# Performance work log

Measured on AMD Instinct MI355X. Metric: run time of the kernel, lower is better.

The kernel has to match this reference:

```python
import jax, jax.numpy as jnp
import numpy as np

N, E = 100000, 1600000
D_IN, D_H, D_OUT = 128, 128, 64


def setup_inputs() -> dict:
    key = jax.random.key(0)
    ks = jax.random.split(key, 9)
    features = jax.random.normal(ks[0], (N, D_IN), dtype=jnp.float32)
    src = jax.random.randint(ks[1], (E,), 0, N, dtype=jnp.int32)
    dst = jax.random.randint(ks[2], (E,), 0, N, dtype=jnp.int32)
    # GraphConv weights (glorot-ish scale)
    W1 = jax.random.normal(ks[3], (D_IN, D_H), dtype=jnp.float32) * (1.0 / np.sqrt(D_IN))
    b1 = jnp.zeros((D_H,), dtype=jnp.float32)
    W2 = jax.random.normal(ks[4], (D_H, D_H), dtype=jnp.float32) * (1.0 / np.sqrt(D_H))
    b2 = jnp.zeros((D_H,), dtype=jnp.float32)
    W3 = jax.random.normal(ks[5], (D_H, D_OUT), dtype=jnp.float32) * (1.0 / np.sqrt(D_H))
    b3 = jnp.zeros((D_OUT,), dtype=jnp.float32)
    return {"features": features, "src": src, "dst": dst,
            "W1": W1, "b1": b1, "W2": W2, "b2": b2, "W3": W3, "b3": b3}


def reference(features, src, dst, W1, b1, W2, b2, W3, b3):
    n = features.shape[0]
    ones_e = jnp.ones(src.shape[0], dtype=features.dtype)
    # DGL GraphConv norm='both': degrees clamped to min 1
    out_deg = jnp.clip(jax.ops.segment_sum(ones_e, src, num_segments=n), 1.0)
    in_deg = jnp.clip(jax.ops.segment_sum(ones_e, dst, num_segments=n), 1.0)
    norm_src = out_deg ** -0.5  # [N]
    norm_dst = in_deg ** -0.5   # [N]

    def graph_conv(h, W, b, relu):
        h = h * norm_src[:, None]                                   # D_out^{-1/2} scale
        m = jax.ops.segment_sum(h[src], dst, num_segments=n)        # SpMM aggregate
        m = m * norm_dst[:, None]                                   # D_in^{-1/2} scale
        h = m @ W + b                                               # linear
        return jax.nn.relu(h) if relu else h

    # dropout is identity in eval mode (deterministic reference)
    h = graph_conv(features, W1, b1, True)
    h = graph_conv(h, W2, b2, True)
    h = graph_conv(h, W3, b3, False)
    return jax.nn.log_softmax(h, axis=1)
```

## Files before the change

### kernel.cpp

```cpp
#include <hip/hip_runtime.h>
#include <math.h>

#define D 128
#define DO 64

#define CHUNK_BITS 15
#define CHUNK_SZ   32768
#define HWORDS     (CHUNK_SZ/4)
#define NSLICE     64

typedef unsigned int uint32;
typedef short bf8s __attribute__((ext_vector_type(8)));
typedef float f32x16 __attribute__((ext_vector_type(16)));

__device__ __forceinline__ unsigned short f2bf(float f) {
    uint32 u = __float_as_uint(f);
    u += 0x7FFFu + ((u >> 16) & 1u);
    return (unsigned short)(u >> 16);
}
__device__ __forceinline__ float bf_lo(uint32 p) { return __uint_as_float(p << 16); }
__device__ __forceinline__ float bf_hi(uint32 p) { return __uint_as_float(p & 0xFFFF0000u); }
__device__ __forceinline__ void acc2(float4& a, uint2 q) {
    a.x += bf_lo(q.x); a.y += bf_hi(q.x);
    a.z += bf_lo(q.y); a.w += bf_hi(q.y);
}

__device__ __forceinline__ f32x16 mfma32(bf8s a, bf8s b, f32x16 c) {
    return __builtin_amdgcn_mfma_f32_32x32x16_bf16(a, b, c, 0, 0, 0);
}
#define ZERO16 {0.f,0.f,0.f,0.f,0.f,0.f,0.f,0.f,0.f,0.f,0.f,0.f,0.f,0.f,0.f,0.f}

__global__ void k_pack_w(const float* __restrict__ W1, const float* __restrict__ W2,
                         const float* __restrict__ W3,
                         unsigned short* __restrict__ P1, unsigned short* __restrict__ P2,
                         unsigned short* __restrict__ P3) {
    int t = blockIdx.x * 256 + threadIdx.x;
    const float* W; unsigned short* P; int slot, NCT, ncols;
    if (t < 2048)      { W = W1; P = P1; slot = t;        NCT = 4; ncols = 128; }
    else if (t < 4096) { W = W2; P = P2; slot = t - 2048; NCT = 4; ncols = 128; }
    else if (t < 5120) { W = W3; P = P3; slot = t - 4096; NCT = 2; ncols = 64;  }
    else return;
    int lane = slot & 63, rest = slot >> 6;
    int ct = rest % NCT, ks = rest / NCT;
    int k0 = ks * 16 + (lane >> 5) * 8;
    int colidx = ct * 32 + (lane & 31);
    unsigned u[4];
#pragma unroll
    for (int b = 0; b < 4; ++b) {
        unsigned lo = f2bf(W[(size_t)(k0 + 2 * b) * ncols + colidx]);
        unsigned hi = f2bf(W[(size_t)(k0 + 2 * b + 1) * ncols + colidx]);
        u[b] = lo | (hi << 16);
    }
    ((uint4*)P)[slot] = make_uint4(u[0], u[1], u[2], u[3]);
}

__global__ __launch_bounds__(256) void k_hist_gemm1(
    const int* __restrict__ src, const int* __restrict__ dst, int E,
    int NH, int NBg, int gemmPer,
    uint32* __restrict__ histS, uint32* __restrict__ histD,
    const float* __restrict__ F, const unsigned short* __restrict__ Wp1,
    unsigned short* __restrict__ T1, int N) {
    __shared__ __align__(16) char smemraw[64 * 132 * 4];
    const int tid = threadIdx.x;
    const int P = 1 + gemmPer;
    const int per = blockIdx.x / P;
    const int pos = blockIdx.x % P;

    if (pos == 0) {
        if (per >= 2 * NH) return;
        bool isS = per >= NH;
        int h = isS ? per - NH : per;
        int chunk = h / NSLICE, slice = h % NSLICE;
        const int* key = isS ? src : dst;
        uint32* hist = (uint32*)smemraw;
        for (int w = tid; w < HWORDS; w += 256) hist[w] = 0;
        __syncthreads();
        int base = chunk << CHUNK_BITS;
        const int nE4 = E >> 2;
        int lo = (int)(((long long)slice * nE4) / NSLICE);
        int hi = (int)(((long long)(slice + 1) * nE4) / NSLICE);
        for (int idx = lo + tid; idx < hi; idx += 256) {
            int4 k4 = ((const int4*)key)[idx];
            unsigned o;
            o = (unsigned)(k4.x - base); if (o < CHUNK_SZ) atomicAdd(&hist[o >> 2], 1u << ((o & 3) * 8));
            o = (unsigned)(k4.y - base); if (o < CHUNK_SZ) atomicAdd(&hist[o >> 2], 1u << ((o & 3) * 8));
            o = (unsigned)(k4.z - base); if (o < CHUNK_SZ) atomicAdd(&hist[o >> 2], 1u << ((o & 3) * 8));
            o = (unsigned)(k4.w - base); if (o < CHUNK_SZ) atomicAdd(&hist[o >> 2], 1u << ((o & 3) * 8));
        }
        if (slice == NSLICE - 1 && tid == 0) {
            for (int i = nE4 * 4; i < E; ++i) {
                unsigned o = (unsigned)(key[i] - base);
                if (o < CHUNK_SZ) atomicAdd(&hist[o >> 2], 1u << ((o & 3) * 8));
            }
        }
        __syncthreads();
        uint32* outp = (isS ? histS : histD) + (size_t)h * HWORDS;
        for (int w = tid; w < HWORDS; w += 256) outp[w] = hist[w];
        return;
    }
    int gid = per * gemmPer + (pos - 1);
    if (gid >= NBg) return;
    const int n0 = gid * 64;
    const float4* M4 = (const float4*)F;
#pragma unroll
    for (int it = 0; it < 8; ++it) {
        int id = it * 256 + tid;
        int nl = id >> 5, k4 = id & 31;
        float4 v = make_float4(0.f, 0.f, 0.f, 0.f);
        int n = n0 + nl;
        if (n < N) v = M4[(size_t)n * 32 + k4];
        ushort4 o;
        o.x = f2bf(v.x); o.y = f2bf(v.y); o.z = f2bf(v.z); o.w = f2bf(v.w);
        *(ushort4*)(smemraw + ((unsigned)(nl * 256 + k4 * 8) ^ ((nl & 15) << 4))) = o;
    }
    __syncthreads();
    const int wid = tid >> 6, wl = tid & 63;
    const int rt = wid >> 1, ctb = (wid & 1) * 2;
    const bf8s* Wp = (const bf8s*)Wp1;
    f32x16 acc0 = ZERO16, acc1 = ZERO16;
    const int arow = rt * 32 + (wl & 31);
    const unsigned axor = (unsigned)((arow & 15) << 4);
    const unsigned abase = (unsigned)(arow * 256 + (wl >> 5) * 16);
#pragma unroll
    for (int ks = 0; ks < 8; ++ks) {
        bf8s af = *(const bf8s*)(smemraw + ((abase + ks * 32) ^ axor));
        acc0 = mfma32(af, Wp[(ks * 4 + ctb) * 64 + wl], acc0);
        acc1 = mfma32(af, Wp[(ks * 4 + ctb + 1) * 64 + wl], acc1);
    }
    const int colb = wl & 31;
    const int rbase = rt * 32 + ((wl >> 5) << 2);
#pragma unroll
    for (int reg = 0; reg < 16; ++reg) {
        int n = n0 + (reg & 3) + 8 * (reg >> 2) + rbase;
        if (n < N) {
            T1[(size_t)n * 128 + ctb * 32 + colb] = f2bf(acc0[reg]);
            T1[(size_t)n * 128 + (ctb + 1) * 32 + colb] = f2bf(acc1[reg]);
        }
    }
}

__global__ void k_merge_norms(const uint32* __restrict__ histS, uint32* __restrict__ histD,
                              int* __restrict__ degi, float* __restrict__ ns,
                              float* __restrict__ nd, int N, int NCHUNK) {
    int w = blockIdx.x * 256 + threadIdx.x;
    if (w >= NCHUNK * HWORDS) return;
    int chunk = w / HWORDS, ww = w - chunk * HWORDS;
    int n0 = (chunk << CHUNK_BITS) + ww * 4;
    if (n0 >= N) return;
    size_t basehist = ((size_t)chunk * NSLICE) * HWORDS + ww;
    uint32 runD = 0, runS = 0;
#pragma unroll 4
    for (int s = 0; s < NSLICE; ++s) {
        size_t idx = basehist + (size_t)s * HWORDS;
        uint32 c = histD[idx];
        histD[idx] = runD;
        runD += c;
        runS += histS[idx];
    }
#pragma unroll
    for (int k = 0; k < 4; ++k) {
        int n = n0 + k;
        if (n < N) {
            int dcur = (int)((runD >> (k * 8)) & 0xFF);
            int ocur = (int)((runS >> (k * 8)) & 0xFF);
            degi[n] = dcur;
            ns[n] = rsqrtf((float)(ocur < 1 ? 1 : ocur));
            nd[n] = rsqrtf((float)(dcur < 1 ? 1 : dcur));
        }
    }
}

__global__ void k_scan_block(const int* __restrict__ cnt, int* __restrict__ rp,
                             int* __restrict__ bsum, int N) {
    __shared__ int sdat[256];
    int i = blockIdx.x * 256 + threadIdx.x;
    int v = (i < N) ? cnt[i] : 0;
    sdat[threadIdx.x] = v;
    __syncthreads();
    for (int off = 1; off < 256; off <<= 1) {
        int t = (threadIdx.x >= off) ? sdat[threadIdx.x - off] : 0;
        __syncthreads();
        sdat[threadIdx.x] += t;
        __syncthreads();
    }
    if (i < N) rp[i] = sdat[threadIdx.x] - v;
    if (threadIdx.x == 255) bsum[blockIdx.x] = sdat[255];
}

__global__ void k_scan_bsum(int* __restrict__ bsum, int NB) {
    __shared__ int sdat[512];
    int tid = threadIdx.x;
    int v = (tid < NB) ? bsum[tid] : 0;
    sdat[tid] = v;
    __syncthreads();
    for (int off = 1; off < 512; off <<= 1) {
        int t = (tid >= off) ? sdat[tid - off] : 0;
        __syncthreads();
        sdat[tid] += t;
        __syncthreads();
    }
    if (tid < NB) bsum[tid] = sdat[tid] - v;
}

__global__ void k_scan_add(int* __restrict__ rp, const int* __restrict__ bsum,
                           int N, int E, uint32* __restrict__ Az, uint32* __restrict__ Bz) {
    int i = blockIdx.x * 256 + threadIdx.x;
    if (i < N) rp[i] += bsum[i >> 8];
    if (i == N) rp[N] = E;
    if (i < 64) { Az[i] = 0; Bz[i] = 0; }
}

__global__ __launch_bounds__(256) void k_scatter_rescale(
    const int* __restrict__ src, const int* __restrict__ dst, int E,
    const uint32* __restrict__ histD, const int* __restrict__ rp,
    int* __restrict__ col, int NH,
    unsigned short* __restrict__ T1, const float* __restrict__ ns, int N) {
    __shared__ uint32 cnt[HWORDS];
    const int tid = threadIdx.x;
    if (blockIdx.x >= NH) {
        int i = (blockIdx.x - NH) * 256 + tid;
        if (i < N * 32) {
            float s = ns[i >> 5];
            uint2 q = ((uint2*)T1)[i];
            ushort4 o;
            o.x = f2bf(bf_lo(q.x) * s); o.y = f2bf(bf_hi(q.x) * s);
            o.z = f2bf(bf_lo(q.y) * s); o.w = f2bf(bf_hi(q.y) * s);
            ((uint2*)T1)[i] = *(uint2*)&o;
        }
        return;
    }
    int chunk = blockIdx.x / NSLICE, slice = blockIdx.x % NSLICE;
    const uint32* Pslice = histD + ((size_t)(chunk * NSLICE + slice)) * HWORDS;
    for (int w = tid; w < HWORDS; w += 256) cnt[w] = Pslice[w];
    __syncthreads();
    int base = chunk << CHUNK_BITS;
    const int nE4 = E >> 2;
    int lo = (int)(((long long)slice * nE4) / NSLICE);
    int hi = (int)(((long long)(slice + 1) * nE4) / NSLICE);
    for (int idx = lo + tid; idx < hi; idx += 256) {
        int4 s4 = ((const int4*)src)[idx];
        int4 d4 = ((const int4*)dst)[idx];
        unsigned o;
        o = (unsigned)(d4.x - base);
        if (o < CHUNK_SZ) {
            uint32 old = atomicAdd(&cnt[o >> 2], 1u << ((o & 3) * 8));
            col[rp[d4.x] + ((old >> ((o & 3) * 8)) & 0xFF)] = s4.x;
        }
        o = (unsigned)(d4.y - base);
        if (o < CHUNK_SZ) {
            uint32 old = atomicAdd(&cnt[o >> 2], 1u << ((o & 3) * 8));
            col[rp[d4.y] + ((old >> ((o & 3) * 8)) & 0xFF)] = s4.y;
        }
        o = (unsigned)(d4.z - base);
        if (o < CHUNK_SZ) {
            uint32 old = atomicAdd(&cnt[o >> 2], 1u << ((o & 3) * 8));
            col[rp[d4.z] + ((old >> ((o & 3) * 8)) & 0xFF)] = s4.z;
        }
        o = (unsigned)(d4.w - base);
        if (o < CHUNK_SZ) {
            uint32 old = atomicAdd(&cnt[o >> 2], 1u << ((o & 3) * 8));
            col[rp[d4.w] + ((old >> ((o & 3) * 8)) & 0xFF)] = s4.w;
        }
    }
    if (slice == NSLICE - 1 && tid == 0) {
        for (int i = nE4 * 4; i < E; ++i) {
            unsigned o = (unsigned)(dst[i] - base);
            if (o < CHUNK_SZ) {
                uint32 old = atomicAdd(&cnt[o >> 2], 1u << ((o & 3) * 8));
                col[rp[dst[i]] + ((old >> ((o & 3) * 8)) & 0xFF)] = src[i];
            }
        }
    }
}


#define SPMM_SH(K) int c##K = __shfl(cvec, j + K, 32);
#define SPMM_LD(K) uint2 q##K = T2[(((unsigned)c##K) << 5) + (unsigned)lane];
#define SPMM_AC(K) acc2(((K) & 1) ? a1 : a0, q##K);

__device__ __forceinline__ float4 spmm_gather_row(
    const uint2* __restrict__ T2, const int* __restrict__ col,
    int s, int e, int cvec, int lane, int N) {
    float4 a0 = make_float4(0.f, 0.f, 0.f, 0.f), a1 = a0;
    int base = s, rem = e - s;
#pragma unroll 1
    while (rem > 0) {
        int cnt = rem < 32 ? rem : 32;
        int padded = (cnt + 7) & ~7;
        int j = 0;
#pragma unroll 1
        for (; j + 16 <= padded; j += 16) {
            SPMM_SH(0) SPMM_SH(1) SPMM_SH(2) SPMM_SH(3)
            SPMM_SH(4) SPMM_SH(5) SPMM_SH(6) SPMM_SH(7)
            SPMM_SH(8) SPMM_SH(9) SPMM_SH(10) SPMM_SH(11)
            SPMM_SH(12) SPMM_SH(13) SPMM_SH(14) SPMM_SH(15)
            SPMM_LD(0) SPMM_LD(1) SPMM_LD(2) SPMM_LD(3)
            SPMM_LD(4) SPMM_LD(5) SPMM_LD(6) SPMM_LD(7)
            SPMM_LD(8) SPMM_LD(9) SPMM_LD(10) SPMM_LD(11)
            SPMM_LD(12) SPMM_LD(13) SPMM_LD(14) SPMM_LD(15)
            SPMM_AC(0) SPMM_AC(1) SPMM_AC(2) SPMM_AC(3)
            SPMM_AC(4) SPMM_AC(5) SPMM_AC(6) SPMM_AC(7)
            SPMM_AC(8) SPMM_AC(9) SPMM_AC(10) SPMM_AC(11)
            SPMM_AC(12) SPMM_AC(13) SPMM_AC(14) SPMM_AC(15)
        }
        if (j < padded) {
            SPMM_SH(0) SPMM_SH(1) SPMM_SH(2) SPMM_SH(3)
            SPMM_SH(4) SPMM_SH(5) SPMM_SH(6) SPMM_SH(7)
            SPMM_LD(0) SPMM_LD(1) SPMM_LD(2) SPMM_LD(3)
            SPMM_LD(4) SPMM_LD(5) SPMM_LD(6) SPMM_LD(7)
            SPMM_AC(0) SPMM_AC(1) SPMM_AC(2) SPMM_AC(3)
            SPMM_AC(4) SPMM_AC(5) SPMM_AC(6) SPMM_AC(7)
        }
        base += 32; rem -= 32;
        if (rem > 0) {
            int t = base + lane;
            cvec = (t < e) ? col[t] : N;
        }
    }
    float4 r;
    r.x = a0.x + a1.x; r.y = a0.y + a1.y;
    r.z = a0.z + a1.z; r.w = a0.w + a1.w;
    return r;
}

#define A64_SH(K) int c##K = __shfl(cvec, j + K, 32);
#define A64_LD(K) uint32 q##K = Y2[(((unsigned)c##K) << 5) + (unsigned)lane];
#define A64_AC(K) { if ((K) & 1) { lo1 += bf_lo(q##K); hi1 += bf_hi(q##K); } \
                    else         { lo0 += bf_lo(q##K); hi0 += bf_hi(q##K); } }

__device__ __forceinline__ float2 agg64_gather_row(
    const uint32* __restrict__ Y2, const int* __restrict__ col,
    int s, int e, int cvec, int lane, int N) {
    float lo0 = 0.f, hi0 = 0.f, lo1 = 0.f, hi1 = 0.f;
    int base = s, rem = e - s;
#pragma unroll 1
    while (rem > 0) {
        int cnt = rem < 32 ? rem : 32;
        int padded = (cnt + 7) & ~7;
        int j = 0;
#pragma unroll 1
        for (; j + 16 <= padded; j += 16) {
            A64_SH(0) A64_SH(1) A64_SH(2) A64_SH(3)
            A64_SH(4) A64_SH(5) A64_SH(6) A64_SH(7)
            A64_SH(8) A64_SH(9) A64_SH(10) A64_SH(11)
            A64_SH(12) A64_SH(13) A64_SH(14) A64_SH(15)
            A64_LD(0) A64_LD(1) A64_LD(2) A64_LD(3)
            A64_LD(4) A64_LD(5) A64_LD(6) A64_LD(7)
            A64_LD(8) A64_LD(9) A64_LD(10) A64_LD(11)
            A64_LD(12) A64_LD(13) A64_LD(14) A64_LD(15)
            A64_AC(0) A64_AC(1) A64_AC(2) A64_AC(3)
            A64_AC(4) A64_AC(5) A64_AC(6) A64_AC(7)
            A64_AC(8) A64_AC(9) A64_AC(10) A64_AC(11)
            A64_AC(12) A64_AC(13) A64_AC(14) A64_AC(15)
        }
        if (j < padded) {
            A64_SH(0) A64_SH(1) A64_SH(2) A64_SH(3)
            A64_SH(4) A64_SH(5) A64_SH(6) A64_SH(7)
            A64_LD(0) A64_LD(1) A64_LD(2) A64_LD(3)
            A64_LD(4) A64_LD(5) A64_LD(6) A64_LD(7)
            A64_AC(0) A64_AC(1) A64_AC(2) A64_AC(3)
            A64_AC(4) A64_AC(5) A64_AC(6) A64_AC(7)
        }
        base += 32; rem -= 32;
        if (rem > 0) {
            int t = base + lane;
            cvec = (t < e) ? col[t] : N;
        }
    }
    return make_float2(lo0 + lo1, hi0 + hi1);
}

template <int JOUT>
__global__ __launch_bounds__(256) void k_spmm_gemm(
    const unsigned short* __restrict__ T, const int* __restrict__ rp,
    const int* __restrict__ col, const float* __restrict__ ns,
    const float* __restrict__ nd, const float* __restrict__ bias,
    const unsigned short* __restrict__ Wpk, unsigned short* __restrict__ out, int N) {
    __shared__ __align__(16) char MsRaw[32 * 256];
    if (JOUT == 64 && blockIdx.x == 0 && threadIdx.x < 32) {
        ((uint32*)out)[(size_t)N * 32 + threadIdx.x] = 0;
    }
    const int n0 = blockIdx.x * 32;
    const int g = threadIdx.x >> 5;
    const int lane = threadIdx.x & 31;
    const uint2* T2 = (const uint2*)T;
    float4 bv = ((const float4*)bias)[lane];

    const int row0 = n0 + (g << 2);
    int rb = 0;
    {
        int idx = row0 + lane;
        if (idx > N) idx = N;
        if (lane < 5) rb = rp[idx];
    }
    int s0 = __shfl(rb, 0, 32), s1 = __shfl(rb, 1, 32), s2 = __shfl(rb, 2, 32),
        s3 = __shfl(rb, 3, 32), s4 = __shfl(rb, 4, 32);
    int cv0 = N, cv1 = N, cv2 = N, cv3 = N;
    { int t = s0 + lane; if (t < s1) cv0 = col[t]; }
    { int t = s1 + lane; if (t < s2) cv1 = col[t]; }
    { int t = s2 + lane; if (t < s3) cv2 = col[t]; }
    { int t = s3 + lane; if (t < s4) cv3 = col[t]; }

#define SPMM_ROW_EPI(RI, SS, EE, CV) { \
    float4 t = spmm_gather_row(T2, col, SS, EE, CV, lane, N); \
    int row = row0 + RI; \
    if (row < N) { \
        float sd = nd[row], sr = ns[row]; \
        ushort4 o; \
        o.x = f2bf(fmaxf(fmaf(t.x, sd, bv.x), 0.f) * sr); \
        o.y = f2bf(fmaxf(fmaf(t.y, sd, bv.y), 0.f) * sr); \
        o.z = f2bf(fmaxf(fmaf(t.z, sd, bv.z), 0.f) * sr); \
        o.w = f2bf(fmaxf(fmaf(t.w, sd, bv.w), 0.f) * sr); \
        int lr = row - n0; \
        *(ushort4*)(MsRaw + ((unsigned)(lr * 256 + lane * 8) ^ ((lr & 15) << 4))) = o; \
    } }

    SPMM_ROW_EPI(0, s0, s1, cv0)
    SPMM_ROW_EPI(1, s1, s2, cv1)
    SPMM_ROW_EPI(2, s2, s3, cv2)
    SPMM_ROW_EPI(3, s3, s4, cv3)
#undef SPMM_ROW_EPI

    __syncthreads();
    const int wid = threadIdx.x >> 6, wl = threadIdx.x & 63;
    const int NCT = (JOUT == 128) ? 4 : 2;
    if (JOUT == 128 || wid < 2) {
        const bf8s* Wp = (const bf8s*)Wpk;
        f32x16 acc = ZERO16;
        const int arow = wl & 31;
        const unsigned axor = (unsigned)((arow & 15) << 4);
        const unsigned abase = (unsigned)(arow * 256 + (wl >> 5) * 16);
#pragma unroll
        for (int ks = 0; ks < 8; ++ks) {
            bf8s af = *(const bf8s*)(MsRaw + ((abase + ks * 32) ^ axor));
            acc = mfma32(af, Wp[(ks * NCT + wid) * 64 + wl], acc);
        }
        const int colb = wid * 32 + (wl & 31);
        const int rb2 = (wl >> 5) << 2;
#pragma unroll
        for (int reg = 0; reg < 16; ++reg) {
            int n = n0 + (reg & 3) + 8 * (reg >> 2) + rb2;
            if (n < N) out[(size_t)n * JOUT + colb] = f2bf(acc[reg]);
        }
    }
}

__global__ __launch_bounds__(256) void k_agg64_lsm(
    const unsigned short* __restrict__ Y, const int* __restrict__ rp,
    const int* __restrict__ col, const float* __restrict__ nd,
    const float* __restrict__ b3, float* __restrict__ out, int N) {
    int row = blockIdx.x * 8 + (threadIdx.x >> 5);
    if (row >= N) return;
    int lane = threadIdx.x & 31;
    const uint32* Y2 = (const uint32*)Y;
    int s = rp[row], e = rp[row + 1];
    int cv;
    { int t = s + lane; cv = (t < e) ? col[t] : N; }
    float2 agg = agg64_gather_row(Y2, col, s, e, cv, lane, N);
    float sd = nd[row];
    float2 bb = ((const float2*)b3)[lane];
    float v0 = agg.x * sd + bb.x;
    float v1 = agg.y * sd + bb.y;
    float m = fmaxf(v0, v1);
#pragma unroll
    for (int o = 16; o; o >>= 1) m = fmaxf(m, __shfl_xor(m, o, 32));
    float ex = expf(v0 - m) + expf(v1 - m);
#pragma unroll
    for (int o = 16; o; o >>= 1) ex += __shfl_xor(ex, o, 32);
    float ls = m + logf(ex);
    ((float2*)out)[(size_t)row * 32 + lane] = make_float2(v0 - ls, v1 - ls);
}

extern "C" void kernel_launch(void* const* d_in, const int* in_sizes, int n_in,
                              void* d_out, int out_size, void* d_ws, size_t ws_size,
                              hipStream_t stream) {
    const float* features = (const float*)d_in[0];
    const int*   src      = (const int*)d_in[1];
    const int*   dst      = (const int*)d_in[2];
    const float* W1       = (const float*)d_in[3];
    const float* b1       = (const float*)d_in[4];
    const float* W2       = (const float*)d_in[5];
    const float* b2       = (const float*)d_in[6];
    const float* W3       = (const float*)d_in[7];
    const float* b3       = (const float*)d_in[8];
    float* out = (float*)d_out;

    const int N = in_sizes[0] / D;
    const int E = in_sizes[1];

    const int NCHUNK = (N + CHUNK_SZ - 1) >> CHUNK_BITS;
    const int NH = NCHUNK * NSLICE;

    char* p = (char*)d_ws;
    unsigned short* A = (unsigned short*)p; p += ((size_t)N + 1) * D * sizeof(unsigned short);
    unsigned short* B = (unsigned short*)p; p += ((size_t)N + 1) * D * sizeof(unsigned short);
    int* col    = (int*)p;   p += (size_t)E * sizeof(int);
    int* rp     = (int*)p;   p += ((size_t)N + 4) * sizeof(int);
    int* degi   = (int*)p;   p += (size_t)N * sizeof(int);
    float* ns   = (float*)p; p += (size_t)N * sizeof(float);
    float* nd   = (float*)p; p += (size_t)N * sizeof(float);
    int* bsum   = (int*)p;   p += 4096 * sizeof(int);
    uint32* histS = (uint32*)p; p += (size_t)NH * HWORDS * sizeof(uint32);
    uint32* histD = (uint32*)p; p += (size_t)NH * HWORDS * sizeof(uint32);
    unsigned short* Wp1 = (unsigned short*)p; p += 16384 * sizeof(unsigned short);
    unsigned short* Wp2 = (unsigned short*)p; p += 16384 * sizeof(unsigned short);
    unsigned short* Wp3 = (unsigned short*)p; p += 8192 * sizeof(unsigned short);

    const int gN  = (N + 255) / 256;
    const int NBg = (N + 63) / 64;
    const int periods = 2 * NH;
    const int gemmPer = (NBg + periods - 1) / periods;
    const int G1 = periods * (1 + gemmPer);

    k_pack_w<<<20, 256, 0, stream>>>(W1, W2, W3, Wp1, Wp2, Wp3);
    k_hist_gemm1<<<G1, 256, 0, stream>>>(src, dst, E, NH, NBg, gemmPer,
                                         histS, histD, features, Wp1, B, N);
    k_merge_norms<<<(NCHUNK * HWORDS + 255) / 256, 256, 0, stream>>>(
        histS, histD, degi, ns, nd, N, NCHUNK);
    k_scan_block<<<gN, 256, 0, stream>>>(degi, rp, bsum, N);
    k_scan_bsum<<<1, 512, 0, stream>>>(bsum, gN);
    k_scan_add<<<(N + 1 + 255) / 256, 256, 0, stream>>>(
        rp, bsum, N, E,
        (uint32*)(A + (size_t)N * D), (uint32*)(B + (size_t)N * D));
    const int RB = (N * 32 + 255) / 256;
    k_scatter_rescale<<<NH + RB, 256, 0, stream>>>(src, dst, E, histD, rp, col, NH,
                                                   B, ns, N);

    const int NBn32 = (N + 31) / 32;
    k_spmm_gemm<128><<<NBn32, 256, 0, stream>>>(B, rp, col, ns, nd, b1, Wp2, A, N);
    k_spmm_gemm<64><<<NBn32, 256, 0, stream>>>(A, rp, col, ns, nd, b2, Wp3, B, N);
    k_agg64_lsm<<<(N + 7) / 8, 256, 0, stream>>>(B, rp, col, nd, b3, out, N);
}
```

Measured before the change: 335.8 us.

## Interleave four-row gathers with double-buffered software-pipelined loads

Replaces the per-row sequential neighbor gather with a routine that walks four rows at once, issuing the next batch of row loads for all four rows into a second register buffer before accumulating the current batch. The aim is to keep more independent global loads in flight per wavefront and hide gather latency. The final aggregation/log-softmax kernel also moves from one row per 32-lane group to four rows per group, using the same interleaved gather. The cost is higher register pressure, which may lower occupancy, plus more control flow when row lengths are uneven.

Result: slower. 395.5 us (+17.8%).

```diff
diff --git a/kernel.cpp b/kernel.cpp
--- a/kernel.cpp
+++ b/kernel.cpp
@@ -274,100 +274,142 @@
 }
 
 
-#define SPMM_SH(K) int c##K = __shfl(cvec, j + K, 32);
-#define SPMM_LD(K) uint2 q##K = T2[(((unsigned)c##K) << 5) + (unsigned)lane];
-#define SPMM_AC(K) acc2(((K) & 1) ? a1 : a0, q##K);
-
-__device__ __forceinline__ float4 spmm_gather_row(
+struct GRow { int base, e, off, cv; };
+
+__device__ __forceinline__ void grow_init(GRow& r, const int* __restrict__ col,
+                                          int s, int e, int lane, int N) {
+    r.base = s; r.e = e; r.off = 0;
+    int t = s + lane;
+    r.cv = (t < e) ? col[t] : N;
+}
+__device__ __forceinline__ void grow_next4(GRow& r, const int* __restrict__ col,
+                                           int lane, int N, int c[4]) {
+#pragma unroll
+    for (int k = 0; k < 4; ++k) c[k] = __shfl(r.cv, r.off + k, 32);
+    r.off += 4;
+    if (r.off == 32) {
+        r.base += 32; r.off = 0;
+        int t = r.base + lane;
+        r.cv = (t < r.e) ? col[t] : N;
+    }
+}
+__device__ __forceinline__ void grow_next8(GRow& r, const int* __restrict__ col,
+                                           int lane, int N, int c[8]) {
+#pragma unroll
+    for (int k = 0; k < 8; ++k) c[k] = __shfl(r.cv, r.off + k, 32);
+    r.off += 8;
+    if (r.off == 32) {
+        r.base += 32; r.off = 0;
+        int t = r.base + lane;
+        r.cv = (t < r.e) ? col[t] : N;
+    }
+}
+
+__device__ __forceinline__ void spmm_quad(
     const uint2* __restrict__ T2, const int* __restrict__ col,
-    int s, int e, int cvec, int lane, int N) {
-    float4 a0 = make_float4(0.f, 0.f, 0.f, 0.f), a1 = a0;
-    int base = s, rem = e - s;
+    int s0, int s1, int s2, int s3, int s4, int lane, int N,
+    float4& t0, float4& t1, float4& t2, float4& t3) {
+    GRow R0, R1, R2, R3;
+    grow_init(R0, col, s0, s1, lane, N);
+    grow_init(R1, col, s1, s2, lane, N);
+    grow_init(R2, col, s2, s3, lane, N);
+    grow_init(R3, col, s3, s4, lane, N);
+    int nb0 = (s1 - s0 + 3) >> 2, nb1 = (s2 - s1 + 3) >> 2;
+    int nb2 = (s3 - s2 + 3) >> 2, nb3 = (s4 - s3 + 3) >> 2;
+    int nb = nb0 > nb1 ? nb0 : nb1;
+    if (nb2 > nb) nb = nb2;
+    if (nb3 > nb) nb = nb3;
+    float4 a0 = make_float4(0.f, 0.f, 0.f, 0.f), a1 = a0, a2 = a0, a3 = a0;
+    uint2 qa0[4], qa1[4], qa2[4], qa3[4];
+    uint2 qb0[4], qb1[4], qb2[4], qb3[4];
+#define ISSQ(R, Q) { int c[4]; grow_next4(R, col, lane, N, c); \
+    _Pragma("unroll") for (int k = 0; k < 4; ++k) \
+        Q[k] = T2[(((unsigned)c[k]) << 5) + (unsigned)lane]; }
+#define CONQ(Q, A) { _Pragma("unroll") for (int k = 0; k < 4; ++k) acc2(A, Q[k]); }
+    if (nb0 > 0) ISSQ(R0, qa0)
+    if (nb1 > 0) ISSQ(R1, qa1)
+    if (nb2 > 0) ISSQ(R2, qa2)
+    if (nb3 > 0) ISSQ(R3, qa3)
+    int i = 0;
 #pragma unroll 1
-    while (rem > 0) {
-        int cnt = rem < 32 ? rem : 32;
-        int padded = (cnt + 7) & ~7;
-        int j = 0;
+    while (i < nb) {
+        if (i + 1 < nb0) ISSQ(R0, qb0)
+        if (i + 1 < nb1) ISSQ(R1, qb1)
+        if (i + 1 < nb2) ISSQ(R2, qb2)
+        if (i + 1 < nb3) ISSQ(R3, qb3)
+        if (i < nb0) CONQ(qa0, a0)
+        if (i < nb1) CONQ(qa1, a1)
+        if (i < nb2) CONQ(qa2, a2)
+        if (i < nb3) CONQ(qa3, a3)
+        ++i;
+        if (i >= nb) break;
+        if (i + 1 < nb0) ISSQ(R0, qa0)
+        if (i + 1 < nb1) ISSQ(R1, qa1)
+        if (i + 1 < nb2) ISSQ(R2, qa2)
+        if (i + 1 < nb3) ISSQ(R3, qa3)
+        if (i < nb0) CONQ(qb0, a0)
+        if (i < nb1) CONQ(qb1, a1)
+        if (i < nb2) CONQ(qb2, a2)
+        if (i < nb3) CONQ(qb3, a3)
+        ++i;
+    }
+#undef ISSQ
+#undef CONQ
+    t0 = a0; t1 = a1; t2 = a2; t3 = a3;
+}
+
+__device__ __forceinline__ void agg_quad(
+    const uint32* __restrict__ Y2, const int* __restrict__ col,
+    int s0, int s1, int s2, int s3, int s4, int lane, int N,
+    float2& t0, float2& t1, float2& t2, float2& t3) {
+    GRow R0, R1, R2, R3;
+    grow_init(R0, col, s0, s1, lane, N);
+    grow_init(R1, col, s1, s2, lane, N);
+    grow_init(R2, col, s2, s3, lane, N);
+    grow_init(R3, col, s3, s4, lane, N);
+    int nb0 = (s1 - s0 + 7) >> 3, nb1 = (s2 - s1 + 7) >> 3;
+    int nb2 = (s3 - s2 + 7) >> 3, nb3 = (s4 - s3 + 7) >> 3;
+    int nb = nb0 > nb1 ? nb0 : nb1;
+    if (nb2 > nb) nb = nb2;
+    if (nb3 > nb) nb = nb3;
+    float2 a0 = make_float2(0.f, 0.f), a1 = a0, a2 = a0, a3 = a0;
+    uint32 qa0[8], qa1[8], qa2[8], qa3[8];
+    uint32 qb0[8], qb1[8], qb2[8], qb3[8];
+#define ISSA(R, Q) { int c[8]; grow_next8(R, col, lane, N, c); \
+    _Pragma("unroll") for (int k = 0; k < 8; ++k) \
+        Q[k] = Y2[(((unsigned)c[k]) << 5) + (unsigned)lane]; }
+#define CONA(Q, A) { _Pragma("unroll") for (int k = 0; k < 8; ++k) { \
+        A.x += bf_lo(Q[k]); A.y += bf_hi(Q[k]); } }
+    if (nb0 > 0) ISSA(R0, qa0)
+    if (nb1 > 0) ISSA(R1, qa1)
+    if (nb2 > 0) ISSA(R2, qa2)
+    if (nb3 > 0) ISSA(R3, qa3)
+    int i = 0;
 #pragma unroll 1
-        for (; j + 16 <= padded; j += 16) {
-            SPMM_SH(0) SPMM_SH(1) SPMM_SH(2) SPMM_SH(3)
-            SPMM_SH(4) SPMM_SH(5) SPMM_SH(6) SPMM_SH(7)
-            SPMM_SH(8) SPMM_SH(9) SPMM_SH(10) SPMM_SH(11)
-            SPMM_SH(12) SPMM_SH(13) SPMM_SH(14) SPMM_SH(15)
-            SPMM_LD(0) SPMM_LD(1) SPMM_LD(2) SPMM_LD(3)
-            SPMM_LD(4) SPMM_LD(5) SPMM_LD(6) SPMM_LD(7)
-            SPMM_LD(8) SPMM_LD(9) SPMM_LD(10) SPMM_LD(11)
-            SPMM_LD(12) SPMM_LD(13) SPMM_LD(14) SPMM_LD(15)
-            SPMM_AC(0) SPMM_AC(1) SPMM_AC(2) SPMM_AC(3)
-            SPMM_AC(4) SPMM_AC(5) SPMM_AC(6) SPMM_AC(7)
-            SPMM_AC(8) SPMM_AC(9) SPMM_AC(10) SPMM_AC(11)
-            SPMM_AC(12) SPMM_AC(13) SPMM_AC(14) SPMM_AC(15)
-        }
-        if (j < padded) {
-            SPMM_SH(0) SPMM_SH(1) SPMM_SH(2) SPMM_SH(3)
-            SPMM_SH(4) SPMM_SH(5) SPMM_SH(6) SPMM_SH(7)
-            SPMM_LD(0) SPMM_LD(1) SPMM_LD(2) SPMM_LD(3)
-            SPMM_LD(4) SPMM_LD(5) SPMM_LD(6) SPMM_LD(7)
-            SPMM_AC(0) SPMM_AC(1) SPMM_AC(2) SPMM_AC(3)
-            SPMM_AC(4) SPMM_AC(5) SPMM_AC(6) SPMM_AC(7)
-        }
-        base += 32; rem -= 32;
-        if (rem > 0) {
-            int t = base + lane;
-            cvec = (t < e) ? col[t] : N;
-        }
-    }
-    float4 r;
-    r.x = a0.x + a1.x; r.y = a0.y + a1.y;
-    r.z = a0.z + a1.z; r.w = a0.w + a1.w;
-    return r;
-}
-
-#define A64_SH(K) int c##K = __shfl(cvec, j + K, 32);
-#define A64_LD(K) uint32 q##K = Y2[(((unsigned)c##K) << 5) + (unsigned)lane];
-#define A64_AC(K) { if ((K) & 1) { lo1 += bf_lo(q##K); hi1 += bf_hi(q##K); } \
-                    else         { lo0 += bf_lo(q##K); hi0 += bf_hi(q##K); } }
-
-__device__ __forceinline__ float2 agg64_gather_row(
-    const uint32* __restrict__ Y2, const int* __restrict__ col,
-    int s, int e, int cvec, int lane, int N) {
-    float lo0 = 0.f, hi0 = 0.f, lo1 = 0.f, hi1 = 0.f;
-    int base = s, rem = e - s;
-#pragma unroll 1
-    while (rem > 0) {
-        int cnt = rem < 32 ? rem : 32;
-        int padded = (cnt + 7) & ~7;
-        int j = 0;
-#pragma unroll 1
-        for (; j + 16 <= padded; j += 16) {
-            A64_SH(0) A64_SH(1) A64_SH(2) A64_SH(3)
-            A64_SH(4) A64_SH(5) A64_SH(6) A64_SH(7)
-            A64_SH(8) A64_SH(9) A64_SH(10) A64_SH(11)
-            A64_SH(12) A64_SH(13) A64_SH(14) A64_SH(15)
-            A64_LD(0) A64_LD(1) A64_LD(2) A64_LD(3)
-            A64_LD(4) A64_LD(5) A64_LD(6) A64_LD(7)
-            A64_LD(8) A64_LD(9) A64_LD(10) A64_LD(11)
-            A64_LD(12) A64_LD(13) A64_LD(14) A64_LD(15)
-            A64_AC(0) A64_AC(1) A64_AC(2) A64_AC(3)
-            A64_AC(4) A64_AC(5) A64_AC(6) A64_AC(7)
-            A64_AC(8) A64_AC(9) A64_AC(10) A64_AC(11)
-            A64_AC(12) A64_AC(13) A64_AC(14) A64_AC(15)
-        }
-        if (j < padded) {
-            A64_SH(0) A64_SH(1) A64_SH(2) A64_SH(3)
-            A64_SH(4) A64_SH(5) A64_SH(6) A64_SH(7)
-            A64_LD(0) A64_LD(1) A64_LD(2) A64_LD(3)
-            A64_LD(4) A64_LD(5) A64_LD(6) A64_LD(7)
-            A64_AC(0) A64_AC(1) A64_AC(2) A64_AC(3)
-            A64_AC(4) A64_AC(5) A64_AC(6) A64_AC(7)
-        }
-        base += 32; rem -= 32;
-        if (rem > 0) {
-            int t = base + lane;
-            cvec = (t < e) ? col[t] : N;
-        }
-    }
-    return make_float2(lo0 + lo1, hi0 + hi1);
+    while (i < nb) {
+        if (i + 1 < nb0) ISSA(R0, qb0)
+        if (i + 1 < nb1) ISSA(R1, qb1)
+        if (i + 1 < nb2) ISSA(R2, qb2)
+        if (i + 1 < nb3) ISSA(R3, qb3)
+        if (i < nb0) CONA(qa0, a0)
+        if (i < nb1) CONA(qa1, a1)
+        if (i < nb2) CONA(qa2, a2)
+        if (i < nb3) CONA(qa3, a3)
+        ++i;
+        if (i >= nb) break;
+        if (i + 1 < nb0) ISSA(R0, qa0)
+        if (i + 1 < nb1) ISSA(R1, qa1)
+        if (i + 1 < nb2) ISSA(R2, qa2)
+        if (i + 1 < nb3) ISSA(R3, qa3)
+        if (i < nb0) CONA(qb0, a0)
+        if (i < nb1) CONA(qb1, a1)
+        if (i < nb2) CONA(qb2, a2)
+        if (i < nb3) CONA(qb3, a3)
+        ++i;
+    }
+#undef ISSA
+#undef CONA
+    t0 = a0; t1 = a1; t2 = a2; t3 = a3;
 }
 
 template <int JOUT>
@@ -395,30 +437,27 @@
     }
     int s0 = __shfl(rb, 0, 32), s1 = __shfl(rb, 1, 32), s2 = __shfl(rb, 2, 32),
         s3 = __shfl(rb, 3, 32), s4 = __shfl(rb, 4, 32);
-    int cv0 = N, cv1 = N, cv2 = N, cv3 = N;
-    { int t = s0 + lane; if (t < s1) cv0 = col[t]; }
-    { int t = s1 + lane; if (t < s2) cv1 = col[t]; }
-    { int t = s2 + lane; if (t < s3) cv2 = col[t]; }
-    { int t = s3 + lane; if (t < s4) cv3 = col[t]; }
-
-#define SPMM_ROW_EPI(RI, SS, EE, CV) { \
-    float4 t = spmm_gather_row(T2, col, SS, EE, CV, lane, N); \
+
+    float4 t0, t1, t2, t3;
+    spmm_quad(T2, col, s0, s1, s2, s3, s4, lane, N, t0, t1, t2, t3);
+
+#define SPMM_ROW_EPI(RI, T_) { \
     int row = row0 + RI; \
     if (row < N) { \
         float sd = nd[row], sr = ns[row]; \
         ushort4 o; \
-        o.x = f2bf(fmaxf(fmaf(t.x, sd, bv.x), 0.f) * sr); \
-        o.y = f2bf(fmaxf(fmaf(t.y, sd, bv.y), 0.f) * sr); \
-        o.z = f2bf(fmaxf(fmaf(t.z, sd, bv.z), 0.f) * sr); \
-        o.w = f2bf(fmaxf(fmaf(t.w, sd, bv.w), 0.f) * sr); \
+        o.x = f2bf(fmaxf(fmaf(T_.x, sd, bv.x), 0.f) * sr); \
+        o.y = f2bf(fmaxf(fmaf(T_.y, sd, bv.y), 0.f) * sr); \
+        o.z = f2bf(fmaxf(fmaf(T_.z, sd, bv.z), 0.f) * sr); \
+        o.w = f2bf(fmaxf(fmaf(T_.w, sd, bv.w), 0.f) * sr); \
         int lr = row - n0; \
         *(ushort4*)(MsRaw + ((unsigned)(lr * 256 + lane * 8) ^ ((lr & 15) << 4))) = o; \
     } }
 
-    SPMM_ROW_EPI(0, s0, s1, cv0)
-    SPMM_ROW_EPI(1, s1, s2, cv1)
-    SPMM_ROW_EPI(2, s2, s3, cv2)
-    SPMM_ROW_EPI(3, s3, s4, cv3)
+    SPMM_ROW_EPI(0, t0)
+    SPMM_ROW_EPI(1, t1)
+    SPMM_ROW_EPI(2, t2)
+    SPMM_ROW_EPI(3, t3)
 #undef SPMM_ROW_EPI
 
     __syncthreads();
@@ -449,26 +488,38 @@
     const unsigned short* __restrict__ Y, const int* __restrict__ rp,
     const int* __restrict__ col, const float* __restrict__ nd,
     const float* __restrict__ b3, float* __restrict__ out, int N) {
-    int row = blockIdx.x * 8 + (threadIdx.x >> 5);
-    if (row >= N) return;
-    int lane = threadIdx.x & 31;
+    const int g = threadIdx.x >> 5;
+    const int lane = threadIdx.x & 31;
+    const int row0 = blockIdx.x * 32 + (g << 2);
     const uint32* Y2 = (const uint32*)Y;
-    int s = rp[row], e = rp[row + 1];
-    int cv;
-    { int t = s + lane; cv = (t < e) ? col[t] : N; }
-    float2 agg = agg64_gather_row(Y2, col, s, e, cv, lane, N);
-    float sd = nd[row];
+    int rb = 0;
+    {
+        int idx = row0 + lane;
+        if (idx > N) idx = N;
+        if (lane < 5) rb = rp[idx];
+    }
+    int s0 = __shfl(rb, 0, 32), s1 = __shfl(rb, 1, 32), s2 = __shfl(rb, 2, 32),
+        s3 = __shfl(rb, 3, 32), s4 = __shfl(rb, 4, 32);
+    float2 t0, t1, t2, t3;
+    agg_quad(Y2, col, s0, s1, s2, s3, s4, lane, N, t0, t1, t2, t3);
     float2 bb = ((const float2*)b3)[lane];
-    float v0 = agg.x * sd + bb.x;
-    float v1 = agg.y * sd + bb.y;
-    float m = fmaxf(v0, v1);
-#pragma unroll
-    for (int o = 16; o; o >>= 1) m = fmaxf(m, __shfl_xor(m, o, 32));
-    float ex = expf(v0 - m) + expf(v1 - m);
-#pragma unroll
-    for (int o = 16; o; o >>= 1) ex += __shfl_xor(ex, o, 32);
-    float ls = m + logf(ex);
-    ((float2*)out)[(size_t)row * 32 + lane] = make_float2(v0 - ls, v1 - ls);
+#define LSM_EPI(RI, T_) { \
+    int row = row0 + RI; \
+    if (row < N) { \
+        float sd = nd[row]; \
+        float v0 = T_.x * sd + bb.x, v1 = T_.y * sd + bb.y; \
+        float m = fmaxf(v0, v1); \
+        _Pragma("unroll") for (int o = 16; o; o >>= 1) m = fmaxf(m, __shfl_xor(m, o, 32)); \
+        float ex = expf(v0 - m) + expf(v1 - m); \
+        _Pragma("unroll") for (int o = 16; o; o >>= 1) ex += __shfl_xor(ex, o, 32); \
+        float ls = m + logf(ex); \
+        ((float2*)out)[(size_t)row * 32 + lane] = make_float2(v0 - ls, v1 - ls); \
+    } }
+    LSM_EPI(0, t0)
+    LSM_EPI(1, t1)
+    LSM_EPI(2, t2)
+    LSM_EPI(3, t3)
+#undef LSM_EPI
 }
 
 extern "C" void kernel_launch(void* const* d_in, const int* in_sizes, int n_in,
@@ -529,5 +580,5 @@
     const int NBn32 = (N + 31) / 32;
     k_spmm_gemm<128><<<NBn32, 256, 0, stream>>>(B, rp, col, ns, nd, b1, Wp2, A, N);
     k_spmm_gemm<64><<<NBn32, 256, 0, stream>>>(A, rp, col, ns, nd, b2, Wp3, B, N);
-    k_agg64_lsm<<<(N + 7) / 8, 256, 0, stream>>>(B, rp, col, nd, b3, out, N);
-}
+    k_agg64_lsm<<<NBn32, 256, 0, stream>>>(B, rp, col, nd, b3, out, N);
+}
```

## Issue first 16 neighbor gathers for four rows up front to raise memory parallelism

Applied to the files above, without the earlier changes.

The SpMM and final aggregation kernels now issue the first 16 neighbor-row loads for all four rows a warp handles before doing any accumulation. This puts many more gathers in flight per wave and hides latency for the average degree of 16. Broadcasts use ds_swizzle instead of __shfl, and the final aggregation kernel moves from one row per 32-lane group to four rows per group, matching the SpMM kernel. Launch bounds gain occupancy hints, and the large prefetch register arrays risk spills or lower occupancy.

After: 358.3 us. 1.07x slower.

```diff
diff --git a/kernel.cpp b/kernel.cpp
--- a/kernel.cpp
+++ b/kernel.cpp
@@ -29,6 +29,8 @@
     return __builtin_amdgcn_mfma_f32_32x32x16_bf16(a, b, c, 0, 0, 0);
 }
 #define ZERO16 {0.f,0.f,0.f,0.f,0.f,0.f,0.f,0.f,0.f,0.f,0.f,0.f,0.f,0.f,0.f,0.f}
+
+#define BC32(V, K) __builtin_amdgcn_ds_swizzle((V), (K) << 5)
 
 __global__ void k_pack_w(const float* __restrict__ W1, const float* __restrict__ W2,
                          const float* __restrict__ W3,
@@ -274,48 +276,68 @@
 }
 
 
-#define SPMM_SH(K) int c##K = __shfl(cvec, j + K, 32);
-#define SPMM_LD(K) uint2 q##K = T2[(((unsigned)c##K) << 5) + (unsigned)lane];
-#define SPMM_AC(K) acc2(((K) & 1) ? a1 : a0, q##K);
-
-__device__ __forceinline__ float4 spmm_gather_row(
+#define ISS16_U2(Q, CV) { \
+    Q[0]  = T2[(((unsigned)BC32(CV, 0))  << 5) + ul]; \
+    Q[1]  = T2[(((unsigned)BC32(CV, 1))  << 5) + ul]; \
+    Q[2]  = T2[(((unsigned)BC32(CV, 2))  << 5) + ul]; \
+    Q[3]  = T2[(((unsigned)BC32(CV, 3))  << 5) + ul]; \
+    Q[4]  = T2[(((unsigned)BC32(CV, 4))  << 5) + ul]; \
+    Q[5]  = T2[(((unsigned)BC32(CV, 5))  << 5) + ul]; \
+    Q[6]  = T2[(((unsigned)BC32(CV, 6))  << 5) + ul]; \
+    Q[7]  = T2[(((unsigned)BC32(CV, 7))  << 5) + ul]; \
+    Q[8]  = T2[(((unsigned)BC32(CV, 8))  << 5) + ul]; \
+    Q[9]  = T2[(((unsigned)BC32(CV, 9))  << 5) + ul]; \
+    Q[10] = T2[(((unsigned)BC32(CV, 10)) << 5) + ul]; \
+    Q[11] = T2[(((unsigned)BC32(CV, 11)) << 5) + ul]; \
+    Q[12] = T2[(((unsigned)BC32(CV, 12)) << 5) + ul]; \
+    Q[13] = T2[(((unsigned)BC32(CV, 13)) << 5) + ul]; \
+    Q[14] = T2[(((unsigned)BC32(CV, 14)) << 5) + ul]; \
+    Q[15] = T2[(((unsigned)BC32(CV, 15)) << 5) + ul]; }
+
+#define GB8_U2(CV, J0) { \
+    uint2 x0 = T2[(((unsigned)BC32(CV, J0+0)) << 5) + ul]; \
+    uint2 x1 = T2[(((unsigned)BC32(CV, J0+1)) << 5) + ul]; \
+    uint2 x2 = T2[(((unsigned)BC32(CV, J0+2)) << 5) + ul]; \
+    uint2 x3 = T2[(((unsigned)BC32(CV, J0+3)) << 5) + ul]; \
+    uint2 x4 = T2[(((unsigned)BC32(CV, J0+4)) << 5) + ul]; \
+    uint2 x5 = T2[(((unsigned)BC32(CV, J0+5)) << 5) + ul]; \
+    uint2 x6 = T2[(((unsigned)BC32(CV, J0+6)) << 5) + ul]; \
+    uint2 x7 = T2[(((unsigned)BC32(CV, J0+7)) << 5) + ul]; \
+    acc2(a0, x0); acc2(a1, x1); acc2(a0, x2); acc2(a1, x3); \
+    acc2(a0, x4); acc2(a1, x5); acc2(a0, x6); acc2(a1, x7); }
+
+__device__ __forceinline__ float4 spmm_finish(
     const uint2* __restrict__ T2, const int* __restrict__ col,
-    int s, int e, int cvec, int lane, int N) {
+    int s, int e, int cvec, int lane, int N, const uint2* qf) {
     float4 a0 = make_float4(0.f, 0.f, 0.f, 0.f), a1 = a0;
-    int base = s, rem = e - s;
+    const unsigned ul = (unsigned)lane;
+#pragma unroll
+    for (int k = 0; k < 16; ++k) acc2((k & 1) ? a1 : a0, qf[k]);
+    int cnt = e - s; if (cnt > 32) cnt = 32;
+    int padded = (cnt + 7) & ~7;
+    if (padded == 32)      { GB8_U2(cvec, 16) GB8_U2(cvec, 24) }
+    else if (padded == 24) { GB8_U2(cvec, 16) }
+    int base = s + 32, rem = e - s - 32;
 #pragma unroll 1
     while (rem > 0) {
-        int cnt = rem < 32 ? rem : 32;
-        int padded = (cnt + 7) & ~7;
-        int j = 0;
+        int t = base + lane;
+        int cv = (t < e) ? col[t] : N;
+        int c2 = rem < 32 ? rem : 32;
+        int p2 = (c2 + 7) & ~7;
 #pragma unroll 1
-        for (; j + 16 <= padded; j += 16) {
-            SPMM_SH(0) SPMM_SH(1) SPMM_SH(2) SPMM_SH(3)
-            SPMM_SH(4) SPMM_SH(5) SPMM_SH(6) SPMM_SH(7)
-            SPMM_SH(8) SPMM_SH(9) SPMM_SH(10) SPMM_SH(11)
-            SPMM_SH(12) SPMM_SH(13) SPMM_SH(14) SPMM_SH(15)
-            SPMM_LD(0) SPMM_LD(1) SPMM_LD(2) SPMM_LD(3)
-            SPMM_LD(4) SPMM_LD(5) SPMM_LD(6) SPMM_LD(7)
-            SPMM_LD(8) SPMM_LD(9) SPMM_LD(10) SPMM_LD(11)
-            SPMM_LD(12) SPMM_LD(13) SPMM_LD(14) SPMM_LD(15)
-            SPMM_AC(0) SPMM_AC(1) SPMM_AC(2) SPMM_AC(3)
-            SPMM_AC(4) SPMM_AC(5) SPMM_AC(6) SPMM_AC(7)
-            SPMM_AC(8) SPMM_AC(9) SPMM_AC(10) SPMM_AC(11)
-            SPMM_AC(12) SPMM_AC(13) SPMM_AC(14) SPMM_AC(15)
-        }
-        if (j < padded) {
-            SPMM_SH(0) SPMM_SH(1) SPMM_SH(2) SPMM_SH(3)
-            SPMM_SH(4) SPMM_SH(5) SPMM_SH(6) SPMM_SH(7)
-            SPMM_LD(0) SPMM_LD(1) SPMM_LD(2) SPMM_LD(3)
-            SPMM_LD(4) SPMM_LD(5) SPMM_LD(6) SPMM_LD(7)
-            SPMM_AC(0) SPMM_AC(1) SPMM_AC(2) SPMM_AC(3)
-            SPMM_AC(4) SPMM_AC(5) SPMM_AC(6) SPMM_AC(7)
+        for (int j = 0; j < p2; j += 8) {
+            uint2 x0 = T2[(((unsigned)__shfl(cv, j+0, 32)) << 5) + ul];
+            uint2 x1 = T2[(((unsigned)__shfl(cv, j+1, 32)) << 5) + ul];
+            uint2 x2 = T2[(((unsigned)__shfl(cv, j+2, 32)) << 5) + ul];
+            uint2 x3 = T2[(((unsigned)__shfl(cv, j+3, 32)) << 5) + ul];
+            uint2 x4 = T2[(((unsigned)__shfl(cv, j+4, 32)) << 5) + ul];
+            uint2 x5 = T2[(((unsigned)__shfl(cv, j+5, 32)) << 5) + ul];
+            uint2 x6 = T2[(((unsigned)__shfl(cv, j+6, 32)) << 5) + ul];
+            uint2 x7 = T2[(((unsigned)__shfl(cv, j+7, 32)) << 5) + ul];
+            acc2(a0, x0); acc2(a1, x1); acc2(a0, x2); acc2(a1, x3);
+            acc2(a0, x4); acc2(a1, x5); acc2(a0, x6); acc2(a1, x7);
         }
         base += 32; rem -= 32;
-        if (rem > 0) {
-            int t = base + lane;
-            cvec = (t < e) ? col[t] : N;
-        }
     }
     float4 r;
     r.x = a0.x + a1.x; r.y = a0.y + a1.y;
@@ -323,55 +345,81 @@
     return r;
 }
 
-#define A64_SH(K) int c##K = __shfl(cvec, j + K, 32);
-#define A64_LD(K) uint32 q##K = Y2[(((unsigned)c##K) << 5) + (unsigned)lane];
-#define A64_AC(K) { if ((K) & 1) { lo1 += bf_lo(q##K); hi1 += bf_hi(q##K); } \
-                    else         { lo0 += bf_lo(q##K); hi0 += bf_hi(q##K); } }
-
-__device__ __forceinline__ float2 agg64_gather_row(
+#define ISS16_U1(Q, CV) { \
+    Q[0]  = Y2[(((unsigned)BC32(CV, 0))  << 5) + ul]; \
+    Q[1]  = Y2[(((unsigned)BC32(CV, 1))  << 5) + ul]; \
+    Q[2]  = Y2[(((unsigned)BC32(CV, 2))  << 5) + ul]; \
+    Q[3]  = Y2[(((unsigned)BC32(CV, 3))  << 5) + ul]; \
+    Q[4]  = Y2[(((unsigned)BC32(CV, 4))  << 5) + ul]; \
+    Q[5]  = Y2[(((unsigned)BC32(CV, 5))  << 5) + ul]; \
+    Q[6]  = Y2[(((unsigned)BC32(CV, 6))  << 5) + ul]; \
+    Q[7]  = Y2[(((unsigned)BC32(CV, 7))  << 5) + ul]; \
+    Q[8]  = Y2[(((unsigned)BC32(CV, 8))  << 5) + ul]; \
+    Q[9]  = Y2[(((unsigned)BC32(CV, 9))  << 5) + ul]; \
+    Q[10] = Y2[(((unsigned)BC32(CV, 10)) << 5) + ul]; \
+    Q[11] = Y2[(((unsigned)BC32(CV, 11)) << 5) + ul]; \
+    Q[12] = Y2[(((unsigned)BC32(CV, 12)) << 5) + ul]; \
+    Q[13] = Y2[(((unsigned)BC32(CV, 13)) << 5) + ul]; \
+    Q[14] = Y2[(((unsigned)BC32(CV, 14)) << 5) + ul]; \
+    Q[15] = Y2[(((unsigned)BC32(CV, 15)) << 5) + ul]; }
+
+#define GB8_U1(CV, J0) { \
+    uint32 x0 = Y2[(((unsigned)BC32(CV, J0+0)) << 5) + ul]; \
+    uint32 x1 = Y2[(((unsigned)BC32(CV, J0+1)) << 5) + ul]; \
+    uint32 x2 = Y2[(((unsigned)BC32(CV, J0+2)) << 5) + ul]; \
+    uint32 x3 = Y2[(((unsigned)BC32(CV, J0+3)) << 5) + ul]; \
+    uint32 x4 = Y2[(((unsigned)BC32(CV, J0+4)) << 5) + ul]; \
+    uint32 x5 = Y2[(((unsigned)BC32(CV, J0+5)) << 5) + ul]; \
+    uint32 x6 = Y2[(((unsigned)BC32(CV, J0+6)) << 5) + ul]; \
+    uint32 x7 = Y2[(((unsigned)BC32(CV, J0+7)) << 5) + ul]; \
+    lo0 += bf_lo(x0); hi0 += bf_hi(x0); lo1 += bf_lo(x1); hi1 += bf_hi(x1); \
+    lo0 += bf_lo(x2); hi0 += bf_hi(x2); lo1 += bf_lo(x3); hi1 += bf_hi(x3); \
+    lo0 += bf_lo(x4); hi0 += bf_hi(x4); lo1 += bf_lo(x5); hi1 += bf_hi(x5); \
+    lo0 += bf_lo(x6); hi0 += bf_hi(x6); lo1 += bf_lo(x7); hi1 += bf_hi(x7); }
+
+__device__ __forceinline__ float2 agg_finish(
     const uint32* __restrict__ Y2, const int* __restrict__ col,
-    int s, int e, int cvec, int lane, int N) {
+    int s, int e, int cvec, int lane, int N, const uint32* qf) {
     float lo0 = 0.f, hi0 = 0.f, lo1 = 0.f, hi1 = 0.f;
-    int base = s, rem = e - s;
+    const unsigned ul = (unsigned)lane;
+#pragma unroll
+    for (int k = 0; k < 16; ++k) {
+        if (k & 1) { lo1 += bf_lo(qf[k]); hi1 += bf_hi(qf[k]); }
+        else       { lo0 += bf_lo(qf[k]); hi0 += bf_hi(qf[k]); }
+    }
+    int cnt = e - s; if (cnt > 32) cnt = 32;
+    int padded = (cnt + 7) & ~7;
+    if (padded == 32)      { GB8_U1(cvec, 16) GB8_U1(cvec, 24) }
+    else if (padded == 24) { GB8_U1(cvec, 16) }
+    int base = s + 32, rem = e - s - 32;
 #pragma unroll 1
     while (rem > 0) {
-        int cnt = rem < 32 ? rem : 32;
-        int padded = (cnt + 7) & ~7;
-        int j = 0;
+        int t = base + lane;
+        int cv = (t < e) ? col[t] : N;
+        int c2 = rem < 32 ? rem : 32;
+        int p2 = (c2 + 7) & ~7;
 #pragma unroll 1
-        for (; j + 16 <= padded; j += 16) {
-            A64_SH(0) A64_SH(1) A64_SH(2) A64_SH(3)
-            A64_SH(4) A64_SH(5) A64_SH(6) A64_SH(7)
-            A64_SH(8) A64_SH(9) A64_SH(10) A64_SH(11)
-            A64_SH(12) A64_SH(13) A64_SH(14) A64_SH(15)
-            A64_LD(0) A64_LD(1) A64_LD(2) A64_LD(3)
-            A64_LD(4) A64_LD(5) A64_LD(6) A64_LD(7)
-            A64_LD(8) A64_LD(9) A64_LD(10) A64_LD(11)
-            A64_LD(12) A64_LD(13) A64_LD(14) A64_LD(15)
-            A64_AC(0) A64_AC(1) A64_AC(2) A64_AC(3)
-            A64_AC(4) A64_AC(5) A64_AC(6) A64_AC(7)
-            A64_AC(8) A64_AC(9) A64_AC(10) A64_AC(11)
-            A64_AC(12) A64_AC(13) A64_AC(14) A64_AC(15)
-        }
-        if (j < padded) {
-            A64_SH(0) A64_SH(1) A64_SH(2) A64_SH(3)
-            A64_SH(4) A64_SH(5) A64_SH(6) A64_SH(7)
-            A64_LD(0) A64_LD(1) A64_LD(2) A64_LD(3)
-            A64_LD(4) A64_LD(5) A64_LD(6) A64_LD(7)
-            A64_AC(0) A64_AC(1) A64_AC(2) A64_AC(3)
-            A64_AC(4) A64_AC(5) A64_AC(6) A64_AC(7)
+        for (int j = 0; j < p2; j += 8) {
+            uint32 x0 = Y2[(((unsigned)__shfl(cv, j+0, 32)) << 5) + ul];
+            uint32 x1 = Y2[(((unsigned)__shfl(cv, j+1, 32)) << 5) + ul];
+            uint32 x2 = Y2[(((unsigned)__shfl(cv, j+2, 32)) << 5) + ul];
+            uint32 x3 = Y2[(((unsigned)__shfl(cv, j+3, 32)) << 5) + ul];
+            uint32 x4 = Y2[(((unsigned)__shfl(cv, j+4, 32)) << 5) + ul];
+            uint32 x5 = Y2[(((unsigned)__shfl(cv, j+5, 32)) << 5) + ul];
+            uint32 x6 = Y2[(((unsigned)__shfl(cv, j+6, 32)) << 5) + ul];
+            uint32 x7 = Y2[(((unsigned)__shfl(cv, j+7, 32)) << 5) + ul];
+            lo0 += bf_lo(x0); hi0 += bf_hi(x0); lo1 += bf_lo(x1); hi1 += bf_hi(x1);
+            lo0 += bf_lo(x2); hi0 += bf_hi(x2); lo1 += bf_lo(x3); hi1 += bf_hi(x3);
+            lo0 += bf_lo(x4); hi0 += bf_hi(x4); lo1 += bf_lo(x5); hi1 += bf_hi(x5);
+            lo0 += bf_lo(x6); hi0 += bf_hi(x6); lo1 += bf_lo(x7); hi1 += bf_hi(x7);
         }
         base += 32; rem -= 32;
-        if (rem > 0) {
-            int t = base + lane;
-            cvec = (t < e) ? col[t] : N;
-        }
     }
     return make_float2(lo0 + lo1, hi0 + hi1);
 }
 
 template <int JOUT>
-__global__ __launch_bounds__(256) void k_spmm_gemm(
+__global__ __launch_bounds__(256, 2) void k_spmm_gemm(
     const unsigned short* __restrict__ T, const int* __restrict__ rp,
     const int* __restrict__ col, const float* __restrict__ ns,
     const float* __restrict__ nd, const float* __restrict__ bias,
@@ -383,6 +431,7 @@
     const int n0 = blockIdx.x * 32;
     const int g = threadIdx.x >> 5;
     const int lane = threadIdx.x & 31;
+    const unsigned ul = (unsigned)lane;
     const uint2* T2 = (const uint2*)T;
     float4 bv = ((const float4*)bias)[lane];
 
@@ -401,8 +450,14 @@
     { int t = s2 + lane; if (t < s3) cv2 = col[t]; }
     { int t = s3 + lane; if (t < s4) cv3 = col[t]; }
 
-#define SPMM_ROW_EPI(RI, SS, EE, CV) { \
-    float4 t = spmm_gather_row(T2, col, SS, EE, CV, lane, N); \
+    uint2 qf0[16], qf1[16], qf2[16], qf3[16];
+    ISS16_U2(qf0, cv0)
+    ISS16_U2(qf1, cv1)
+    ISS16_U2(qf2, cv2)
+    ISS16_U2(qf3, cv3)
+
+#define SPMM_ROW_EPI(RI, SS, EE, CV, QF) { \
+    float4 t = spmm_finish(T2, col, SS, EE, CV, lane, N, QF); \
     int row = row0 + RI; \
     if (row < N) { \
         float sd = nd[row], sr = ns[row]; \
@@ -415,10 +470,10 @@
         *(ushort4*)(MsRaw + ((unsigned)(lr * 256 + lane * 8) ^ ((lr & 15) << 4))) = o; \
     } }
 
-    SPMM_ROW_EPI(0, s0, s1, cv0)
-    SPMM_ROW_EPI(1, s1, s2, cv1)
-    SPMM_ROW_EPI(2, s2, s3, cv2)
-    SPMM_ROW_EPI(3, s3, s4, cv3)
+    SPMM_ROW_EPI(0, s0, s1, cv0, qf0)
+    SPMM_ROW_EPI(1, s1, s2, cv1, qf1)
+    SPMM_ROW_EPI(2, s2, s3, cv2, qf2)
+    SPMM_ROW_EPI(3, s3, s4, cv3, qf3)
 #undef SPMM_ROW_EPI
 
     __syncthreads();
@@ -445,30 +500,58 @@
     }
 }
 
-__global__ __launch_bounds__(256) void k_agg64_lsm(
+__global__ __launch_bounds__(256, 3) void k_agg64_lsm(
     const unsigned short* __restrict__ Y, const int* __restrict__ rp,
     const int* __restrict__ col, const float* __restrict__ nd,
     const float* __restrict__ b3, float* __restrict__ out, int N) {
-    int row = blockIdx.x * 8 + (threadIdx.x >> 5);
-    if (row >= N) return;
-    int lane = threadIdx.x & 31;
+    const int g = threadIdx.x >> 5;
+    const int lane = threadIdx.x & 31;
+    const unsigned ul = (unsigned)lane;
+    const int row0 = blockIdx.x * 32 + (g << 2);
     const uint32* Y2 = (const uint32*)Y;
-    int s = rp[row], e = rp[row + 1];
-    int cv;
-    { int t = s + lane; cv = (t < e) ? col[t] : N; }
-    float2 agg = agg64_gather_row(Y2, col, s, e, cv, lane, N);
-    float sd = nd[row];
+    int rb = 0;
+    {
+        int idx = row0 + lane;
+        if (idx > N) idx = N;
+        if (lane < 5) rb = rp[idx];
+    }
+    int s0 = __shfl(rb, 0, 32), s1 = __shfl(rb, 1, 32), s2 = __shfl(rb, 2, 32),
+        s3 = __shfl(rb, 3, 32), s4 = __shfl(rb, 4, 32);
+    int cv0 = N, cv1 = N, cv2 = N, cv3 = N;
+    { int t = s0 + lane; if (t < s1) cv0 = col[t]; }
+    { int t = s1 + lane; if (t < s2) cv1 = col[t]; }
+    { int t = s2 + lane; if (t < s3) cv2 = col[t]; }
+    { int t = s3 + lane; if (t < s4) cv3 = col[t]; }
+
+    uint32 qf0[16], qf1[16], qf2[16], qf3[16];
+    ISS16_U1(qf0, cv0)
+    ISS16_U1(qf1, cv1)
+    ISS16_U1(qf2, cv2)
+    ISS16_U1(qf3, cv3)
+
+    float2 t0 = agg_finish(Y2, col, s0, s1, cv0, lane, N, qf0);
+    float2 t1 = agg_finish(Y2, col, s1, s2, cv1, lane, N, qf1);
+    float2 t2 = agg_finish(Y2, col, s2, s3, cv2, lane, N, qf2);
+    float2 t3 = agg_finish(Y2, col, s3, s4, cv3, lane, N, qf3);
+
     float2 bb = ((const float2*)b3)[lane];
-    float v0 = agg.x * sd + bb.x;
-    float v1 = agg.y * sd + bb.y;
-    float m = fmaxf(v0, v1);
-#pragma unroll
-    for (int o = 16; o; o >>= 1) m = fmaxf(m, __shfl_xor(m, o, 32));
-    float ex = expf(v0 - m) + expf(v1 - m);
-#pragma unroll
-    for (int o = 16; o; o >>= 1) ex += __shfl_xor(ex, o, 32);
-    float ls = m + logf(ex);
-    ((float2*)out)[(size_t)row * 32 + lane] = make_float2(v0 - ls, v1 - ls);
+#define LSM_EPI(RI, T_) { \
+    int row = row0 + RI; \
+    if (row < N) { \
+        float sd = nd[row]; \
+        float v0 = T_.x * sd + bb.x, v1 = T_.y * sd + bb.y; \
+        float m = fmaxf(v0, v1); \
+        _Pragma("unroll") for (int o = 16; o; o >>= 1) m = fmaxf(m, __shfl_xor(m, o, 32)); \
+        float ex = expf(v0 - m) + expf(v1 - m); \
+        _Pragma("unroll") for (int o = 16; o; o >>= 1) ex += __shfl_xor(ex, o, 32); \
+        float ls = m + logf(ex); \
+        ((float2*)out)[(size_t)row * 32 + lane] = make_float2(v0 - ls, v1 - ls); \
+    } }
+    LSM_EPI(0, t0)
+    LSM_EPI(1, t1)
+    LSM_EPI(2, t2)
+    LSM_EPI(3, t3)
+#undef LSM_EPI
 }
 
 extern "C" void kernel_launch(void* const* d_in, const int* in_sizes, int n_in,
@@ -529,5 +612,5 @@
     const int NBn32 = (N + 31) / 32;
     k_spmm_gemm<128><<<NBn32, 256, 0, stream>>>(B, rp, col, ns, nd, b1, Wp2, A, N);
     k_spmm_gemm<64><<<NBn32, 256, 0, stream>>>(A, rp, col, ns, nd, b2, Wp3, B, N);
-    k_agg64_lsm<<<(N + 7) / 8, 256, 0, stream>>>(B, rp, col, nd, b3, out, N);
-}
+    k_agg64_lsm<<<NBn32, 256, 0, stream>>>(B, rp, col, nd, b3, out, N);
+}
```
